# Kernel optimization log

Measured on AMD Instinct MI355X. Metric: run time of the kernel, lower is better.

## Reference

```python
import jax, jax.numpy as jnp
import numpy as np

N = 50000
E = 1600000
D = 128
H = 16  # SE hidden = int(128 * 0.125)
EPS = 1e-5


def _layernorm(x, gamma, beta):
    mu = jnp.mean(x, axis=-1, keepdims=True)
    var = jnp.mean(jnp.square(x - mu), axis=-1, keepdims=True)
    return (x - mu) * jax.lax.rsqrt(var + EPS) * gamma + beta


def _gcn_conv(x, W, b, src, dst):
    # PyG GCNConv, improved=True: self-loop weight 2.0, symmetric norm.
    xw = x @ W                                        # [N, D]
    deg = jax.ops.segment_sum(jnp.ones((E,), x.dtype), dst, num_segments=N) + 2.0
    dinv = jnp.where(deg > 0, jax.lax.rsqrt(deg), 0.0)  # [N]
    norm = dinv[src] * dinv[dst]                      # [E]
    agg = jax.ops.segment_sum(xw[src] * norm[:, None], dst, num_segments=N)
    agg = agg + xw * (2.0 * dinv * dinv)[:, None]     # self-loop contribution
    return agg + b


def setup_inputs() -> dict:
    key = jax.random.key(0)
    ks = jax.random.split(key, 10)
    scale = 1.0 / np.sqrt(D)
    inp = {
        "x": jax.random.normal(ks[0], (N, D), jnp.float32),
        "edge_index": jax.random.randint(ks[1], (2, E), 0, N, jnp.int64),
        "W1": jax.random.normal(ks[2], (D, D), jnp.float32) * scale,
        "b1": jnp.zeros((D,), jnp.float32),
        "g1": jnp.ones((D,), jnp.float32),
        "beta1": jnp.zeros((D,), jnp.float32),
        "W2": jax.random.normal(ks[3], (D, D), jnp.float32) * scale,
        "b2": jnp.zeros((D,), jnp.float32),
        "g2": jnp.ones((D,), jnp.float32),
        "beta2": jnp.zeros((D,), jnp.float32),
        "Ws": jax.random.normal(ks[4], (D, H), jnp.float32) * scale,
        "bs": jnp.zeros((H,), jnp.float32),
        "We": jax.random.normal(ks[5], (H, D), jnp.float32) * (1.0 / np.sqrt(H)),
        "be": jnp.zeros((D,), jnp.float32),
    }
    return inp


def reference(x, edge_index, W1, b1, g1, beta1, W2, b2, g2, beta2, Ws, bs, We, be):
    src, dst = edge_index[0], edge_index[1]
    skip = x
    h = jax.nn.relu(_layernorm(_gcn_conv(x, W1, b1, src, dst), g1, beta1))
    h = _layernorm(_gcn_conv(h, W2, b2, src, dst), g2, beta2)
    # SE gating
    s = jax.nn.relu(h @ Ws + bs)
    w = jax.nn.sigmoid(s @ We + be)
    h = h * w
    return jax.nn.relu(h + skip)
```

## Files before the change

### kernel.cpp

```cpp
#include <hip/hip_runtime.h>
#include <hip/hip_fp16.h>
#include <math.h>

#define DD 128
#define HH 16
#define EPSV 1e-5f

static __device__ __forceinline__ ushort f2bf(float f) {
  uint u = __float_as_uint(f);
  u += 0x7FFFu + ((u >> 16) & 1u);
  return (ushort)(u >> 16);
}
static __device__ __forceinline__ float bflo(uint u) { return __uint_as_float(u << 16); }
static __device__ __forceinline__ float bfhi(uint u) { return __uint_as_float(u & 0xFFFF0000u); }


#define SCAN_T 1024
#define SCAN_I 4

__global__ void k_scan1(const int* __restrict__ deg, int* __restrict__ bsum, int n) {
  __shared__ int sh[SCAN_T];
  int tid = threadIdx.x;
  int base = blockIdx.x * SCAN_T * SCAN_I + tid * SCAN_I;
  int s = 0;
#pragma unroll
  for (int j = 0; j < SCAN_I; ++j) { int i = base + j; if (i < n) s += deg[i]; }
  sh[tid] = s;
  __syncthreads();
  for (int off = SCAN_T / 2; off > 0; off >>= 1) {
    if (tid < off) sh[tid] += sh[tid + off];
    __syncthreads();
  }
  if (tid == 0) bsum[blockIdx.x] = sh[0];
}

__global__ void k_scan2(const int* __restrict__ deg, const int* __restrict__ bsum,
                        int* __restrict__ rowoff, int* __restrict__ cursor,
                        float* __restrict__ dinv, int n) {
  __shared__ int sh[SCAN_T];
  __shared__ int sbase;
  int tid = threadIdx.x;
  int b = blockIdx.x;
  if (tid == 0) { int s = 0; for (int j = 0; j < b; ++j) s += bsum[j]; sbase = s; }
  int base = b * SCAN_T * SCAN_I + tid * SCAN_I;
  int d[SCAN_I]; int ts = 0;
#pragma unroll
  for (int j = 0; j < SCAN_I; ++j) { int i = base + j; d[j] = (i < n) ? deg[i] : 0; ts += d[j]; }
  sh[tid] = ts;
  __syncthreads();
  for (int off = 1; off < SCAN_T; off <<= 1) {
    int v = (tid >= off) ? sh[tid - off] : 0;
    __syncthreads();
    sh[tid] += v;
    __syncthreads();
  }
  int ex = sbase + sh[tid] - ts;
#pragma unroll
  for (int j = 0; j < SCAN_I; ++j) {
    int i = base + j;
    if (i < n) {
      rowoff[i] = ex;
      cursor[i] = ex;
      dinv[i] = rsqrtf((float)d[j] + 2.0f);
    }
    ex += d[j];
  }
}

__global__ void k_fill(const int* __restrict__ src, const int* __restrict__ dst,
                       const float* __restrict__ dinv, int* __restrict__ cursor,
                       uint* __restrict__ csr, int ecnt) {
  int e = blockIdx.x * blockDim.x + threadIdx.x;
  if (e >= ecnt) return;
  int s = src[e], d = dst[e];
  int idx = atomicAdd(&cursor[d], 1);
  float nw = dinv[s] * dinv[d];
  uint hb = (uint)__half_as_ushort(__float2half_rn(nw));
  __builtin_nontemporal_store((hb << 16) | (uint)s, &csr[idx]);
}


static __device__ __forceinline__ void gemm_f32_body(
    const float* __restrict__ A, const float* __restrict__ B,
    ushort* __restrict__ C, int nrows, int bx, float* Bs) {
  int tid = threadIdx.x;
  int tx = tid & 15, ty = tid >> 4;
  int rowbase = (bx >> 1) * 128;
  int c0 = (bx & 1) * 64;
  {
    int kk = tid >> 4;
    int cc = (tid & 15) * 4;
#pragma unroll
    for (int p = 0; p < 8; ++p) {
      int k = p * 16 + kk;
      float4 bv = *reinterpret_cast<const float4*>(&B[k * DD + c0 + cc]);
      *reinterpret_cast<float4*>(&Bs[k * 64 + cc]) = bv;
    }
  }
  __syncthreads();
  float acc[8][4];
#pragma unroll
  for (int i = 0; i < 8; ++i)
#pragma unroll
    for (int j = 0; j < 4; ++j) acc[i][j] = 0.f;
  int rl[8];
#pragma unroll
  for (int i = 0; i < 8; ++i) {
    int r = rowbase + ty * 8 + i;
    rl[i] = (r < nrows) ? r : (nrows - 1);
  }
  const float4* A4 = reinterpret_cast<const float4*>(A);
  for (int kq = 0; kq < 32; ++kq) {
    float4 av[8];
#pragma unroll
    for (int i = 0; i < 8; ++i) av[i] = A4[(size_t)rl[i] * 32 + kq];
#pragma unroll
    for (int j = 0; j < 4; ++j) {
      float4 bv = *reinterpret_cast<const float4*>(&Bs[(kq * 4 + j) * 64 + tx * 4]);
#pragma unroll
      for (int i = 0; i < 8; ++i) {
        float a = (j == 0) ? av[i].x : (j == 1) ? av[i].y : (j == 2) ? av[i].z : av[i].w;
        acc[i][0] = fmaf(a, bv.x, acc[i][0]);
        acc[i][1] = fmaf(a, bv.y, acc[i][1]);
        acc[i][2] = fmaf(a, bv.z, acc[i][2]);
        acc[i][3] = fmaf(a, bv.w, acc[i][3]);
      }
    }
  }
  int cbase = c0 + tx * 4;
#pragma unroll
  for (int i = 0; i < 8; ++i) {
    int r = rowbase + ty * 8 + i;
    if (r < nrows) {
      ushort4 o;
      o.x = f2bf(acc[i][0]); o.y = f2bf(acc[i][1]);
      o.z = f2bf(acc[i][2]); o.w = f2bf(acc[i][3]);
      *reinterpret_cast<ushort4*>(&C[(size_t)r * DD + cbase]) = o;
    }
  }
}

__global__ __launch_bounds__(256) void k_gemm1_hist(
    const float* __restrict__ A, const float* __restrict__ B, ushort* __restrict__ C,
    int nrows, const int* __restrict__ dst, int* __restrict__ deg, int ecnt,
    int gblocks, int hblocks) {
  __shared__ float Bs[DD * 64];
  int bx = blockIdx.x;
  if (bx < gblocks) {
    gemm_f32_body(A, B, C, nrows, bx, Bs);
  } else {
    int hb = bx - gblocks;
    int stride = hblocks * 256;
    for (int e = hb * 256 + threadIdx.x; e < ecnt; e += stride)
      atomicAdd(&deg[dst[e]], 1);
  }
}


__global__ __launch_bounds__(256) void k_gemmb(const ushort* __restrict__ A,
                                               const float* __restrict__ B,
                                               ushort* __restrict__ C, int nrows) {
  __shared__ float Bs[DD * 64];
  int tid = threadIdx.x;
  int tx = tid & 15, ty = tid >> 4;
  int rowbase = (blockIdx.x >> 1) * 128;
  int c0 = (blockIdx.x & 1) * 64;
  {
    int kk = tid >> 4;
    int cc = (tid & 15) * 4;
#pragma unroll
    for (int p = 0; p < 8; ++p) {
      int k = p * 16 + kk;
      float4 bv = *reinterpret_cast<const float4*>(&B[k * DD + c0 + cc]);
      *reinterpret_cast<float4*>(&Bs[k * 64 + cc]) = bv;
    }
  }
  __syncthreads();
  float acc[8][4];
#pragma unroll
  for (int i = 0; i < 8; ++i)
#pragma unroll
    for (int j = 0; j < 4; ++j) acc[i][j] = 0.f;
  int rl[8];
#pragma unroll
  for (int i = 0; i < 8; ++i) {
    int r = rowbase + ty * 8 + i;
    rl[i] = (r < nrows) ? r : (nrows - 1);
  }
  const uint4* A16 = reinterpret_cast<const uint4*>(A);
  for (int kq = 0; kq < 16; ++kq) {
    uint4 av[8];
#pragma unroll
    for (int i = 0; i < 8; ++i) av[i] = A16[(size_t)rl[i] * 16 + kq];
#pragma unroll
    for (int kk = 0; kk < 8; ++kk) {
      float4 bv = *reinterpret_cast<const float4*>(&Bs[(kq * 8 + kk) * 64 + tx * 4]);
#pragma unroll
      for (int i = 0; i < 8; ++i) {
        uint w = (kk < 2) ? av[i].x : (kk < 4) ? av[i].y : (kk < 6) ? av[i].z : av[i].w;
        float a = (kk & 1) ? bfhi(w) : bflo(w);
        acc[i][0] = fmaf(a, bv.x, acc[i][0]);
        acc[i][1] = fmaf(a, bv.y, acc[i][1]);
        acc[i][2] = fmaf(a, bv.z, acc[i][2]);
        acc[i][3] = fmaf(a, bv.w, acc[i][3]);
      }
    }
  }
  int cbase = c0 + tx * 4;
#pragma unroll
  for (int i = 0; i < 8; ++i) {
    int r = rowbase + ty * 8 + i;
    if (r < nrows) {
      ushort4 o;
      o.x = f2bf(acc[i][0]); o.y = f2bf(acc[i][1]);
      o.z = f2bf(acc[i][2]); o.w = f2bf(acc[i][3]);
      *reinterpret_cast<ushort4*>(&C[(size_t)r * DD + cbase]) = o;
    }
  }
}


static __device__ __forceinline__ void edge_accum(
    const uint* __restrict__ xw32, const uint* __restrict__ csr,
    int start, int cnt, uint lane, float& acc0, float& acc1) {
  const uint* cs = csr + __builtin_amdgcn_readfirstlane(start);
  int rem = __builtin_amdgcn_readfirstlane(cnt);
  uint c[8];
  if (rem >= 8) {
#pragma unroll
    for (int j = 0; j < 8; ++j) c[j] = cs[j];
    cs += 8;
  }
  while (rem >= 16) {
    uint v[8];
#pragma unroll
    for (int j = 0; j < 8; ++j) v[j] = xw32[((c[j] & 0xFFFFu) << 6) + lane];
    uint cn[8];
#pragma unroll
    for (int j = 0; j < 8; ++j) cn[j] = cs[j];
#pragma unroll
    for (int j = 0; j < 8; ++j) {
      float nw = __half2float(__ushort_as_half((ushort)(c[j] >> 16)));
      acc0 = fmaf(bflo(v[j]), nw, acc0);
      acc1 = fmaf(bfhi(v[j]), nw, acc1);
    }
#pragma unroll
    for (int j = 0; j < 8; ++j) c[j] = cn[j];
    cs += 8; rem -= 8;
  }
  if (rem >= 8) {
    uint v[8];
#pragma unroll
    for (int j = 0; j < 8; ++j) v[j] = xw32[((c[j] & 0xFFFFu) << 6) + lane];
#pragma unroll
    for (int j = 0; j < 8; ++j) {
      float nw = __half2float(__ushort_as_half((ushort)(c[j] >> 16)));
      acc0 = fmaf(bflo(v[j]), nw, acc0);
      acc1 = fmaf(bfhi(v[j]), nw, acc1);
    }
    rem -= 8;
  }
  if (rem > 0) {
    uint ct[8];
#pragma unroll
    for (int j = 0; j < 8; ++j) ct[j] = cs[j < rem ? j : 0];
    uint v[8];
#pragma unroll
    for (int j = 0; j < 8; ++j) v[j] = xw32[((ct[j] & 0xFFFFu) << 6) + lane];
#pragma unroll
    for (int j = 0; j < 8; ++j) {
      float nw = (j < rem) ? __half2float(__ushort_as_half((ushort)(ct[j] >> 16))) : 0.f;
      acc0 = fmaf(bflo(v[j]), nw, acc0);
      acc1 = fmaf(bfhi(v[j]), nw, acc1);
    }
  }
}


__global__ __launch_bounds__(256) void k_agg1(
    const ushort* __restrict__ xw, const uint* __restrict__ csr,
    const int* __restrict__ rowoff, const int* __restrict__ deg,
    const float* __restrict__ dinv, const float* __restrict__ bias,
    const float* __restrict__ gam, const float* __restrict__ bet,
    uint* __restrict__ outp, int n) {
  int wv = threadIdx.x >> 6, lane = threadIdx.x & 63;
  int i = blockIdx.x * 4 + wv;
  if (i >= n) return;
  int start = rowoff[i], cnt = deg[i];
  float di = dinv[i];
  const uint* xw32 = (const uint*)xw;
  float2 bv = ((const float2*)bias)[lane];
  uint su = xw32[((uint)i << 6) + lane];
  float sw = 2.f * di * di;
  float acc0 = fmaf(bflo(su), sw, bv.x);
  float acc1 = fmaf(bfhi(su), sw, bv.y);
  edge_accum(xw32, csr, start, cnt, (uint)lane, acc0, acc1);
  float s = acc0 + acc1;
#pragma unroll
  for (int off = 32; off > 0; off >>= 1) s += __shfl_xor(s, off);
  float mu = s * (1.f / DD);
  float c0 = acc0 - mu, c1 = acc1 - mu;
  float q = c0 * c0 + c1 * c1;
#pragma unroll
  for (int off = 32; off > 0; off >>= 1) q += __shfl_xor(q, off);
  float rstd = rsqrtf(q * (1.f / DD) + EPSV);
  float2 gv = ((const float2*)gam)[lane];
  float2 tv = ((const float2*)bet)[lane];
  float h0 = fmaxf(fmaf(c0 * rstd, gv.x, tv.x), 0.f);
  float h1 = fmaxf(fmaf(c1 * rstd, gv.y, tv.y), 0.f);
  uint packed = (uint)f2bf(h0) | ((uint)f2bf(h1) << 16);
  __builtin_nontemporal_store(packed, &outp[((uint)i << 6) + lane]);
}


__global__ __launch_bounds__(256) void k_agg2(
    const ushort* __restrict__ xw, const uint* __restrict__ csr,
    const int* __restrict__ rowoff, const int* __restrict__ deg,
    const float* __restrict__ dinv, const float* __restrict__ bias,
    const float* __restrict__ gam, const float* __restrict__ bet,
    const float* __restrict__ Ws, const float* __restrict__ bs,
    const float* __restrict__ We, const float* __restrict__ be,
    const float* __restrict__ xin, float* __restrict__ outp, int n) {
  int wv = threadIdx.x >> 6, lane = threadIdx.x & 63;
  int i = blockIdx.x * 4 + wv;
  if (i >= n) return;
  int start = rowoff[i], cnt = deg[i];
  float di = dinv[i];
  const uint* xw32 = (const uint*)xw;
  float2 bv = ((const float2*)bias)[lane];
  uint su = xw32[((uint)i << 6) + lane];
  float sw = 2.f * di * di;
  float acc0 = fmaf(bflo(su), sw, bv.x);
  float acc1 = fmaf(bfhi(su), sw, bv.y);
  edge_accum(xw32, csr, start, cnt, (uint)lane, acc0, acc1);
  float s = acc0 + acc1;
#pragma unroll
  for (int off = 32; off > 0; off >>= 1) s += __shfl_xor(s, off);
  float mu = s * (1.f / DD);
  float c0 = acc0 - mu, c1 = acc1 - mu;
  float q = c0 * c0 + c1 * c1;
#pragma unroll
  for (int off = 32; off > 0; off >>= 1) q += __shfl_xor(q, off);
  float rstd = rsqrtf(q * (1.f / DD) + EPSV);
  float2 gv = ((const float2*)gam)[lane];
  float2 tv = ((const float2*)bet)[lane];
  float h0 = fmaf(c0 * rstd, gv.x, tv.x);
  float h1 = fmaf(c1 * rstd, gv.y, tv.y);
  float pj[HH];
  const float* wr0 = &Ws[(2 * lane) * HH];
  const float* wr1 = &Ws[(2 * lane + 1) * HH];
#pragma unroll
  for (int j = 0; j < HH; ++j) pj[j] = h0 * wr0[j] + h1 * wr1[j];
#pragma unroll
  for (int off = 32; off > 0; off >>= 1) {
#pragma unroll
    for (int j = 0; j < HH; ++j) pj[j] += __shfl_xor(pj[j], off);
  }
  float2 bev = ((const float2*)be)[lane];
  float wacc0 = bev.x, wacc1 = bev.y;
#pragma unroll
  for (int j = 0; j < HH; ++j) {
    float sj = fmaxf(pj[j] + bs[j], 0.f);
    float2 wev = ((const float2*)(We + j * DD))[lane];
    wacc0 = fmaf(sj, wev.x, wacc0);
    wacc1 = fmaf(sj, wev.y, wacc1);
  }
  float w0 = 1.f / (1.f + __expf(-wacc0));
  float w1 = 1.f / (1.f + __expf(-wacc1));
  float2 xr = ((const float2*)(xin + (size_t)i * DD))[lane];
  float2 o;
  o.x = fmaxf(fmaf(h0, w0, xr.x), 0.f);
  o.y = fmaxf(fmaf(h1, w1, xr.y), 0.f);
  ((float2*)(outp + (size_t)i * DD))[lane] = o;
}


extern "C" void kernel_launch(void* const* d_in, const int* in_sizes, int n_in,
                              void* d_out, int out_size, void* d_ws, size_t ws_size,
                              hipStream_t stream) {
  const float* x   = (const float*)d_in[0];
  const int*   ei  = (const int*)d_in[1];
  const float* W1  = (const float*)d_in[2];
  const float* b1  = (const float*)d_in[3];
  const float* g1  = (const float*)d_in[4];
  const float* be1 = (const float*)d_in[5];
  const float* W2  = (const float*)d_in[6];
  const float* b2  = (const float*)d_in[7];
  const float* g2  = (const float*)d_in[8];
  const float* be2 = (const float*)d_in[9];
  const float* Ws  = (const float*)d_in[10];
  const float* bs  = (const float*)d_in[11];
  const float* We  = (const float*)d_in[12];
  const float* bee = (const float*)d_in[13];
  float* outp = (float*)d_out;

  int n    = in_sizes[0] / DD;
  int ecnt = in_sizes[1] / 2;
  const int* src = ei;
  const int* dst = ei + ecnt;

  char* w = (char*)d_ws;
  ushort* xw    = (ushort*)w; w += (size_t)n * DD * 2;
  uint*   h1    = (uint*)w;   w += (size_t)n * DD * 2;
  int*    deg   = (int*)w;    w += (size_t)n * 4;
  int*    cursor= (int*)w;    w += (size_t)n * 4;
  int*    rowoff= (int*)w;    w += (size_t)n * 4;
  float*  dinv  = (float*)w;  w += (size_t)n * 4;
  int*    bsum  = (int*)w;    w += 64 * 4;
  uint*   csr   = (uint*)w;   w += ((size_t)ecnt + 16) * 4;

  hipMemsetAsync(deg, 0, (size_t)n * 4, stream);

  const int TB = 256;
  int gblocks = ((n + 127) / 128) * 2;
  int hblocks = 2048;
  k_gemm1_hist<<<gblocks + hblocks, TB, 0, stream>>>(x, W1, xw, n, dst, deg, ecnt,
                                                     gblocks, hblocks);
  int nb = (n + SCAN_T * SCAN_I - 1) / (SCAN_T * SCAN_I);
  k_scan1<<<nb, SCAN_T, 0, stream>>>(deg, bsum, n);
  k_scan2<<<nb, SCAN_T, 0, stream>>>(deg, bsum, rowoff, cursor, dinv, n);
  int eb = (ecnt + TB - 1) / TB;
  k_fill<<<eb, TB, 0, stream>>>(src, dst, dinv, cursor, csr, ecnt);

  int nb4 = (n + 3) / 4;
  k_agg1<<<nb4, TB, 0, stream>>>(xw, csr, rowoff, deg, dinv, b1, g1, be1, h1, n);
  k_gemmb<<<gblocks, TB, 0, stream>>>((const ushort*)h1, W2, xw, n);
  k_agg2<<<nb4, TB, 0, stream>>>(xw, csr, rowoff, deg, dinv, b2, g2, be2,
                                 Ws, bs, We, bee, x, outp, n);
}
```

Before: 372.0 us.

## Prescale GEMM rows by dinv and pack CSR as padded 16-bit indices

```diff
diff --git a/kernel.cpp b/kernel.cpp
--- a/kernel.cpp
+++ b/kernel.cpp
@@ -1,5 +1,4 @@
 #include <hip/hip_runtime.h>
-#include <hip/hip_fp16.h>
 #include <math.h>
 
 #define DD 128
@@ -13,6 +12,13 @@
 }
 static __device__ __forceinline__ float bflo(uint u) { return __uint_as_float(u << 16); }
 static __device__ __forceinline__ float bfhi(uint u) { return __uint_as_float(u & 0xFFFF0000u); }
+
+
+__global__ void k_hist(const int* __restrict__ dst, int* __restrict__ deg, int ecnt) {
+  int stride = gridDim.x * blockDim.x;
+  for (int e = blockIdx.x * blockDim.x + threadIdx.x; e < ecnt; e += stride)
+    atomicAdd(&deg[dst[e]], 1);
+}
 
 
 #define SCAN_T 1024
@@ -24,7 +30,10 @@
   int base = blockIdx.x * SCAN_T * SCAN_I + tid * SCAN_I;
   int s = 0;
 #pragma unroll
-  for (int j = 0; j < SCAN_I; ++j) { int i = base + j; if (i < n) s += deg[i]; }
+  for (int j = 0; j < SCAN_I; ++j) {
+    int i = base + j;
+    if (i < n) s += (deg[i] + 7) & ~7;
+  }
   sh[tid] = s;
   __syncthreads();
   for (int off = SCAN_T / 2; off > 0; off >>= 1) {
@@ -36,16 +45,21 @@
 
 __global__ void k_scan2(const int* __restrict__ deg, const int* __restrict__ bsum,
                         int* __restrict__ rowoff, int* __restrict__ cursor,
-                        float* __restrict__ dinv, int n) {
+                        float* __restrict__ dinv, ushort* __restrict__ csr, int n) {
   __shared__ int sh[SCAN_T];
   __shared__ int sbase;
   int tid = threadIdx.x;
   int b = blockIdx.x;
   if (tid == 0) { int s = 0; for (int j = 0; j < b; ++j) s += bsum[j]; sbase = s; }
   int base = b * SCAN_T * SCAN_I + tid * SCAN_I;
-  int d[SCAN_I]; int ts = 0;
-#pragma unroll
-  for (int j = 0; j < SCAN_I; ++j) { int i = base + j; d[j] = (i < n) ? deg[i] : 0; ts += d[j]; }
+  int d[SCAN_I], dp[SCAN_I]; int ts = 0;
+#pragma unroll
+  for (int j = 0; j < SCAN_I; ++j) {
+    int i = base + j;
+    d[j] = (i < n) ? deg[i] : 0;
+    dp[j] = (d[j] + 7) & ~7;
+    ts += dp[j];
+  }
   sh[tid] = ts;
   __syncthreads();
   for (int off = 1; off < SCAN_T; off <<= 1) {
@@ -62,27 +76,18 @@
       rowoff[i] = ex;
       cursor[i] = ex;
       dinv[i] = rsqrtf((float)d[j] + 2.0f);
-    }
-    ex += d[j];
-  }
-}
-
-__global__ void k_fill(const int* __restrict__ src, const int* __restrict__ dst,
-                       const float* __restrict__ dinv, int* __restrict__ cursor,
-                       uint* __restrict__ csr, int ecnt) {
-  int e = blockIdx.x * blockDim.x + threadIdx.x;
-  if (e >= ecnt) return;
-  int s = src[e], d = dst[e];
-  int idx = atomicAdd(&cursor[d], 1);
-  float nw = dinv[s] * dinv[d];
-  uint hb = (uint)__half_as_ushort(__float2half_rn(nw));
-  __builtin_nontemporal_store((hb << 16) | (uint)s, &csr[idx]);
+      for (int k = d[j]; k < dp[j]; ++k) csr[ex + k] = (ushort)n;
+    }
+    ex += dp[j];
+    if (i == n - 1) rowoff[n] = ex;
+  }
 }
 
 
 static __device__ __forceinline__ void gemm_f32_body(
     const float* __restrict__ A, const float* __restrict__ B,
-    ushort* __restrict__ C, int nrows, int bx, float* Bs) {
+    const float* __restrict__ dinv, ushort* __restrict__ C, int nrows, int bx,
+    float* Bs) {
   int tid = threadIdx.x;
   int tx = tid & 15, ty = tid >> 4;
   int rowbase = (bx >> 1) * 128;
@@ -132,33 +137,39 @@
   for (int i = 0; i < 8; ++i) {
     int r = rowbase + ty * 8 + i;
     if (r < nrows) {
+      float dv = dinv[r];
       ushort4 o;
-      o.x = f2bf(acc[i][0]); o.y = f2bf(acc[i][1]);
-      o.z = f2bf(acc[i][2]); o.w = f2bf(acc[i][3]);
+      o.x = f2bf(acc[i][0] * dv); o.y = f2bf(acc[i][1] * dv);
+      o.z = f2bf(acc[i][2] * dv); o.w = f2bf(acc[i][3] * dv);
       *reinterpret_cast<ushort4*>(&C[(size_t)r * DD + cbase]) = o;
     }
   }
 }
 
-__global__ __launch_bounds__(256) void k_gemm1_hist(
-    const float* __restrict__ A, const float* __restrict__ B, ushort* __restrict__ C,
-    int nrows, const int* __restrict__ dst, int* __restrict__ deg, int ecnt,
-    int gblocks, int hblocks) {
+__global__ __launch_bounds__(256) void k_gemm1_fill(
+    const float* __restrict__ A, const float* __restrict__ B,
+    const float* __restrict__ dinv, ushort* __restrict__ C, int nrows,
+    const int* __restrict__ src, const int* __restrict__ dst,
+    int* __restrict__ cursor, ushort* __restrict__ csr, int ecnt,
+    int gblocks, int fblocks) {
   __shared__ float Bs[DD * 64];
   int bx = blockIdx.x;
   if (bx < gblocks) {
-    gemm_f32_body(A, B, C, nrows, bx, Bs);
+    gemm_f32_body(A, B, dinv, C, nrows, bx, Bs);
   } else {
-    int hb = bx - gblocks;
-    int stride = hblocks * 256;
-    for (int e = hb * 256 + threadIdx.x; e < ecnt; e += stride)
-      atomicAdd(&deg[dst[e]], 1);
+    int stride = fblocks * 256;
+    for (int e = (bx - gblocks) * 256 + threadIdx.x; e < ecnt; e += stride) {
+      int s = src[e], d = dst[e];
+      int idx = atomicAdd(&cursor[d], 1);
+      __builtin_nontemporal_store((ushort)s, &csr[idx]);
+    }
   }
 }
 
 
 __global__ __launch_bounds__(256) void k_gemmb(const ushort* __restrict__ A,
                                                const float* __restrict__ B,
+                                               const float* __restrict__ dinv,
                                                ushort* __restrict__ C, int nrows) {
   __shared__ float Bs[DD * 64];
   int tid = threadIdx.x;
@@ -211,9 +222,10 @@
   for (int i = 0; i < 8; ++i) {
     int r = rowbase + ty * 8 + i;
     if (r < nrows) {
+      float dv = dinv[r];
       ushort4 o;
-      o.x = f2bf(acc[i][0]); o.y = f2bf(acc[i][1]);
-      o.z = f2bf(acc[i][2]); o.w = f2bf(acc[i][3]);
+      o.x = f2bf(acc[i][0] * dv); o.y = f2bf(acc[i][1] * dv);
+      o.z = f2bf(acc[i][2] * dv); o.w = f2bf(acc[i][3] * dv);
       *reinterpret_cast<ushort4*>(&C[(size_t)r * DD + cbase]) = o;
     }
   }
@@ -221,85 +233,71 @@
 
 
 static __device__ __forceinline__ void edge_accum(
-    const uint* __restrict__ xw32, const uint* __restrict__ csr,
+    const uint* __restrict__ xw32, const ushort* __restrict__ csr,
     int start, int cnt, uint lane, float& acc0, float& acc1) {
-  const uint* cs = csr + __builtin_amdgcn_readfirstlane(start);
+  const uint4* cs = (const uint4*)(csr + __builtin_amdgcn_readfirstlane(start));
   int rem = __builtin_amdgcn_readfirstlane(cnt);
-  uint c[8];
-  if (rem >= 8) {
-#pragma unroll
-    for (int j = 0; j < 8; ++j) c[j] = cs[j];
-    cs += 8;
-  }
+  uint4 c;
+  if (rem >= 8) c = *cs++;
   while (rem >= 16) {
     uint v[8];
-#pragma unroll
-    for (int j = 0; j < 8; ++j) v[j] = xw32[((c[j] & 0xFFFFu) << 6) + lane];
-    uint cn[8];
-#pragma unroll
-    for (int j = 0; j < 8; ++j) cn[j] = cs[j];
+    v[0] = xw32[((c.x & 0xFFFFu) << 6) + lane];
+    v[1] = xw32[((c.x >> 16) << 6) + lane];
+    v[2] = xw32[((c.y & 0xFFFFu) << 6) + lane];
+    v[3] = xw32[((c.y >> 16) << 6) + lane];
+    v[4] = xw32[((c.z & 0xFFFFu) << 6) + lane];
+    v[5] = xw32[((c.z >> 16) << 6) + lane];
+    v[6] = xw32[((c.w & 0xFFFFu) << 6) + lane];
+    v[7] = xw32[((c.w >> 16) << 6) + lane];
+    uint4 cn = *cs++;
 #pragma unroll
     for (int j = 0; j < 8; ++j) {
-      float nw = __half2float(__ushort_as_half((ushort)(c[j] >> 16)));
-      acc0 = fmaf(bflo(v[j]), nw, acc0);
-      acc1 = fmaf(bfhi(v[j]), nw, acc1);
-    }
-#pragma unroll
-    for (int j = 0; j < 8; ++j) c[j] = cn[j];
-    cs += 8; rem -= 8;
+      acc0 += bflo(v[j]);
+      acc1 += bfhi(v[j]);
+    }
+    c = cn; rem -= 8;
   }
   if (rem >= 8) {
     uint v[8];
-#pragma unroll
-    for (int j = 0; j < 8; ++j) v[j] = xw32[((c[j] & 0xFFFFu) << 6) + lane];
+    v[0] = xw32[((c.x & 0xFFFFu) << 6) + lane];
+    v[1] = xw32[((c.x >> 16) << 6) + lane];
+    v[2] = xw32[((c.y & 0xFFFFu) << 6) + lane];
+    v[3] = xw32[((c.y >> 16) << 6) + lane];
+    v[4] = xw32[((c.z & 0xFFFFu) << 6) + lane];
+    v[5] = xw32[((c.z >> 16) << 6) + lane];
+    v[6] = xw32[((c.w & 0xFFFFu) << 6) + lane];
+    v[7] = xw32[((c.w >> 16) << 6) + lane];
 #pragma unroll
     for (int j = 0; j < 8; ++j) {
-      float nw = __half2float(__ushort_as_half((ushort)(c[j] >> 16)));
-      acc0 = fmaf(bflo(v[j]), nw, acc0);
-      acc1 = fmaf(bfhi(v[j]), nw, acc1);
-    }
-    rem -= 8;
-  }
-  if (rem > 0) {
-    uint ct[8];
-#pragma unroll
-    for (int j = 0; j < 8; ++j) ct[j] = cs[j < rem ? j : 0];
-    uint v[8];
-#pragma unroll
-    for (int j = 0; j < 8; ++j) v[j] = xw32[((ct[j] & 0xFFFFu) << 6) + lane];
-#pragma unroll
-    for (int j = 0; j < 8; ++j) {
-      float nw = (j < rem) ? __half2float(__ushort_as_half((ushort)(ct[j] >> 16))) : 0.f;
-      acc0 = fmaf(bflo(v[j]), nw, acc0);
-      acc1 = fmaf(bfhi(v[j]), nw, acc1);
+      acc0 += bflo(v[j]);
+      acc1 += bfhi(v[j]);
     }
   }
 }
 
 
 __global__ __launch_bounds__(256) void k_agg1(
-    const ushort* __restrict__ xw, const uint* __restrict__ csr,
-    const int* __restrict__ rowoff, const int* __restrict__ deg,
-    const float* __restrict__ dinv, const float* __restrict__ bias,
-    const float* __restrict__ gam, const float* __restrict__ bet,
-    uint* __restrict__ outp, int n) {
+    const ushort* __restrict__ xwd, const ushort* __restrict__ csr,
+    const int* __restrict__ rowoff, const float* __restrict__ dinv,
+    const float* __restrict__ bias, const float* __restrict__ gam,
+    const float* __restrict__ bet, uint* __restrict__ outp, int n) {
   int wv = threadIdx.x >> 6, lane = threadIdx.x & 63;
   int i = blockIdx.x * 4 + wv;
   if (i >= n) return;
-  int start = rowoff[i], cnt = deg[i];
+  int start = rowoff[i], cnt = rowoff[i + 1] - start;
   float di = dinv[i];
-  const uint* xw32 = (const uint*)xw;
+  const uint* xw32 = (const uint*)xwd;
+  float acc0 = 0.f, acc1 = 0.f;
+  edge_accum(xw32, csr, start, cnt, (uint)lane, acc0, acc1);
+  uint su = xw32[((uint)i << 6) + lane];
   float2 bv = ((const float2*)bias)[lane];
-  uint su = xw32[((uint)i << 6) + lane];
-  float sw = 2.f * di * di;
-  float acc0 = fmaf(bflo(su), sw, bv.x);
-  float acc1 = fmaf(bfhi(su), sw, bv.y);
-  edge_accum(xw32, csr, start, cnt, (uint)lane, acc0, acc1);
-  float s = acc0 + acc1;
+  float c0v = fmaf(di, acc0 + 2.f * bflo(su), bv.x);
+  float c1v = fmaf(di, acc1 + 2.f * bfhi(su), bv.y);
+  float s = c0v + c1v;
 #pragma unroll
   for (int off = 32; off > 0; off >>= 1) s += __shfl_xor(s, off);
   float mu = s * (1.f / DD);
-  float c0 = acc0 - mu, c1 = acc1 - mu;
+  float c0 = c0v - mu, c1 = c1v - mu;
   float q = c0 * c0 + c1 * c1;
 #pragma unroll
   for (int off = 32; off > 0; off >>= 1) q += __shfl_xor(q, off);
@@ -314,30 +312,30 @@
 
 
 __global__ __launch_bounds__(256) void k_agg2(
-    const ushort* __restrict__ xw, const uint* __restrict__ csr,
-    const int* __restrict__ rowoff, const int* __restrict__ deg,
-    const float* __restrict__ dinv, const float* __restrict__ bias,
-    const float* __restrict__ gam, const float* __restrict__ bet,
-    const float* __restrict__ Ws, const float* __restrict__ bs,
-    const float* __restrict__ We, const float* __restrict__ be,
-    const float* __restrict__ xin, float* __restrict__ outp, int n) {
+    const ushort* __restrict__ xwd, const ushort* __restrict__ csr,
+    const int* __restrict__ rowoff, const float* __restrict__ dinv,
+    const float* __restrict__ bias, const float* __restrict__ gam,
+    const float* __restrict__ bet, const float* __restrict__ Ws,
+    const float* __restrict__ bs, const float* __restrict__ We,
+    const float* __restrict__ be, const float* __restrict__ xin,
+    float* __restrict__ outp, int n) {
   int wv = threadIdx.x >> 6, lane = threadIdx.x & 63;
   int i = blockIdx.x * 4 + wv;
   if (i >= n) return;
-  int start = rowoff[i], cnt = deg[i];
+  int start = rowoff[i], cnt = rowoff[i + 1] - start;
   float di = dinv[i];
-  const uint* xw32 = (const uint*)xw;
+  const uint* xw32 = (const uint*)xwd;
+  float acc0 = 0.f, acc1 = 0.f;
+  edge_accum(xw32, csr, start, cnt, (uint)lane, acc0, acc1);
+  uint su = xw32[((uint)i << 6) + lane];
   float2 bv = ((const float2*)bias)[lane];
-  uint su = xw32[((uint)i << 6) + lane];
-  float sw = 2.f * di * di;
-  float acc0 = fmaf(bflo(su), sw, bv.x);
-  float acc1 = fmaf(bfhi(su), sw, bv.y);
-  edge_accum(xw32, csr, start, cnt, (uint)lane, acc0, acc1);
-  float s = acc0 + acc1;
+  float c0v = fmaf(di, acc0 + 2.f * bflo(su), bv.x);
+  float c1v = fmaf(di, acc1 + 2.f * bfhi(su), bv.y);
+  float s = c0v + c1v;
 #pragma unroll
   for (int off = 32; off > 0; off >>= 1) s += __shfl_xor(s, off);
   float mu = s * (1.f / DD);
-  float c0 = acc0 - mu, c1 = acc1 - mu;
+  float c0 = c0v - mu, c1 = c1v - mu;
   float q = c0 * c0 + c1 * c1;
 #pragma unroll
   for (int off = 32; off > 0; off >>= 1) q += __shfl_xor(q, off);
@@ -400,31 +398,33 @@
   const int* dst = ei + ecnt;
 
   char* w = (char*)d_ws;
-  ushort* xw    = (ushort*)w; w += (size_t)n * DD * 2;
+  ushort* xwd   = (ushort*)w; w += (size_t)(n + 1) * DD * 2;
   uint*   h1    = (uint*)w;   w += (size_t)n * DD * 2;
   int*    deg   = (int*)w;    w += (size_t)n * 4;
   int*    cursor= (int*)w;    w += (size_t)n * 4;
-  int*    rowoff= (int*)w;    w += (size_t)n * 4;
+  int*    rowoff= (int*)w;    w += (size_t)(n + 1) * 4;
   float*  dinv  = (float*)w;  w += (size_t)n * 4;
   int*    bsum  = (int*)w;    w += 64 * 4;
-  uint*   csr   = (uint*)w;   w += ((size_t)ecnt + 16) * 4;
+  w = (char*)(((size_t)w + 15) & ~(size_t)15);
+  ushort* csr   = (ushort*)w; w += ((size_t)ecnt + 8 * (size_t)n + 16) * 2;
 
   hipMemsetAsync(deg, 0, (size_t)n * 4, stream);
+  hipMemsetAsync(xwd + (size_t)n * DD, 0, DD * 2, stream);
 
   const int TB = 256;
-  int gblocks = ((n + 127) / 128) * 2;
-  int hblocks = 2048;
-  k_gemm1_hist<<<gblocks + hblocks, TB, 0, stream>>>(x, W1, xw, n, dst, deg, ecnt,
-                                                     gblocks, hblocks);
+  k_hist<<<2048, TB, 0, stream>>>(dst, deg, ecnt);
   int nb = (n + SCAN_T * SCAN_I - 1) / (SCAN_T * SCAN_I);
   k_scan1<<<nb, SCAN_T, 0, stream>>>(deg, bsum, n);
-  k_scan2<<<nb, SCAN_T, 0, stream>>>(deg, bsum, rowoff, cursor, dinv, n);
-  int eb = (ecnt + TB - 1) / TB;
-  k_fill<<<eb, TB, 0, stream>>>(src, dst, dinv, cursor, csr, ecnt);
-
+  k_scan2<<<nb, SCAN_T, 0, stream>>>(deg, bsum, rowoff, cursor, dinv, csr, n);
+
+  int gblocks = ((n + 127) / 128) * 2;
+  int fblocks = 2048;
+  k_gemm1_fill<<<gblocks + fblocks, TB, 0, stream>>>(x, W1, dinv, xwd, n,
+                                                     src, dst, cursor, csr, ecnt,
+                                                     gblocks, fblocks);
   int nb4 = (n + 3) / 4;
-  k_agg1<<<nb4, TB, 0, stream>>>(xw, csr, rowoff, deg, dinv, b1, g1, be1, h1, n);
-  k_gemmb<<<gblocks, TB, 0, stream>>>((const ushort*)h1, W2, xw, n);
-  k_agg2<<<nb4, TB, 0, stream>>>(xw, csr, rowoff, deg, dinv, b2, g2, be2,
+  k_agg1<<<nb4, TB, 0, stream>>>(xwd, csr, rowoff, dinv, b1, g1, be1, h1, n);
+  k_gemmb<<<gblocks, TB, 0, stream>>>((const ushort*)h1, W2, dinv, xwd, n);
+  k_agg2<<<nb4, TB, 0, stream>>>(xwd, csr, rowoff, dinv, b2, g2, be2,
                                  Ws, bs, We, bee, x, outp, n);
 }
```

New measurement: 442.7 us. 1.19x slower.
